# Kernel optimization log

Hardware: AMD Instinct MI355X
Metric: run time of the kernel (lower is better)

The kernel has to match this reference:

```python
import jax, jax.numpy as jnp
import numpy as np

NEG_SLOPE = 0.2  # PyG GATConv default negative_slope
N_NODES = 10000
N_EDGES = 320000
IN_CH = 512
HID = 128
HEADS = 4
N_CLASSES = 2


def gat_conv(x, src, dst, n, W, att_src, att_dst, bias, concat):
    """PyG-style GATConv (shared weights for src/dst, eval mode: no dropout)."""
    H, C = att_src.shape
    h = (x @ W).reshape(-1, H, C)                      # [N, H, C]
    a_src = jnp.sum(h * att_src[None], axis=-1)        # [N, H]
    a_dst = jnp.sum(h * att_dst[None], axis=-1)        # [N, H]
    e = a_src[src] + a_dst[dst]                        # [E, H]
    e = jnp.where(e > 0, e, NEG_SLOPE * e)             # LeakyReLU
    # numerically stable softmax over incoming edges of each dst node
    m = jax.ops.segment_max(e, dst, num_segments=n)    # [N, H]
    m = jnp.where(jnp.isfinite(m), m, 0.0)
    ex = jnp.exp(e - m[dst])
    denom = jax.ops.segment_sum(ex, dst, num_segments=n)
    alpha = ex / (denom[dst] + 1e-16)                  # [E, H]
    out = jax.ops.segment_sum(alpha[:, :, None] * h[src], dst, num_segments=n)  # [N,H,C]
    if concat:
        out = out.reshape(n, H * C)
    else:
        out = out.mean(axis=1)
    return out + bias


def setup_inputs() -> dict:
    key = jax.random.key(0)
    ks = jax.random.split(key, 8)
    x = jax.random.normal(ks[0], (N_NODES, IN_CH), dtype=jnp.float32)
    edge_index = jax.random.randint(ks[1], (2, N_EDGES), 0, N_NODES, dtype=jnp.int32)
    s1 = 1.0 / np.sqrt(IN_CH)
    s2 = 1.0 / np.sqrt(HEADS * HID)
    return {
        "x": x,
        "edge_index": edge_index,
        "W1": jax.random.normal(ks[2], (IN_CH, HEADS * HID), dtype=jnp.float32) * s1,
        "att_src1": jax.random.normal(ks[3], (HEADS, HID), dtype=jnp.float32) * s2,
        "att_dst1": jax.random.normal(ks[4], (HEADS, HID), dtype=jnp.float32) * s2,
        "b1": jnp.zeros((HEADS * HID,), dtype=jnp.float32),
        "W2": jax.random.normal(ks[5], (HEADS * HID, N_CLASSES), dtype=jnp.float32) * s2,
        "att_src2": jax.random.normal(ks[6], (1, N_CLASSES), dtype=jnp.float32),
        "att_dst2": jax.random.normal(ks[7], (1, N_CLASSES), dtype=jnp.float32),
        "b2": jnp.zeros((N_CLASSES,), dtype=jnp.float32),
    }


def reference(x, edge_index, W1, att_src1, att_dst1, b1, W2, att_src2, att_dst2, b2):
    n = x.shape[0]
    loop = jnp.arange(n, dtype=edge_index.dtype)       # PyG add_self_loops=True
    src = jnp.concatenate([edge_index[0], loop])
    dst = jnp.concatenate([edge_index[1], loop])
    h = gat_conv(x, src, dst, n, W1, att_src1, att_dst1, b1, concat=True)
    h = jax.nn.elu(h)
    out = gat_conv(h, src, dst, n, W2, att_src2, att_dst2, b2, concat=False)
    return out
```

## Files before the change

### kernel.cpp

```cpp
#include <hip/hip_runtime.h>
#include <hip/hip_bf16.h>

#define N_NODES 10000
#define N_EDGES 320000
#define E_TOT   330000
#define IN_CH   512
#define F1      512
#define HID     128
#define HEADS   4
#define SLOTS   128

typedef __attribute__((ext_vector_type(8))) short bf16x8;
typedef __attribute__((ext_vector_type(4))) float f32x4;

__device__ __forceinline__ float lo16(unsigned u) { return __uint_as_float(u << 16); }
__device__ __forceinline__ float hi16(unsigned u) { return __uint_as_float(u & 0xffff0000u); }
__device__ __forceinline__ unsigned short bfbits(float f) {
    __hip_bfloat16 h = __float2bfloat16(f);
    return *(unsigned short*)&h;
}

__global__ void k_prep(const float* __restrict__ x, unsigned short* __restrict__ xb,
                       const float* __restrict__ w1, unsigned short* __restrict__ w1t,
                       int* __restrict__ zbase,
                       const int* __restrict__ src, const int* __restrict__ dst,
                       int* __restrict__ cnt, int* __restrict__ slots) {
    __shared__ float tile[64][65];
    int b = blockIdx.x;
    int t = threadIdx.x;
    if (b < 5000) {
        int idx = b * 256 + t;
        float4 v = ((const float4*)x)[idx];
        ushort4 u;
        u.x = bfbits(v.x); u.y = bfbits(v.y); u.z = bfbits(v.z); u.w = bfbits(v.w);
        ((ushort4*)xb)[idx] = u;
    } else if (b < 5064) {
        int bb = b - 5000;
        int bi = bb >> 3, bj = bb & 7;
        int r0 = t >> 6, col = t & 63;
#pragma unroll
        for (int p = 0; p < 16; ++p) {
            int row = p * 4 + r0;
            tile[row][col] = w1[(size_t)(bi * 64 + row) * 512 + bj * 64 + col];
        }
        __syncthreads();
#pragma unroll
        for (int p = 0; p < 16; ++p) {
            int row = p * 4 + r0;
            w1t[(size_t)(bj * 64 + row) * 512 + bi * 64 + col] = bfbits(tile[col][row]);
        }
    } else if (b < 5377) {
        int idx = (b - 5064) * 256 + t;
        if (idx < 80000) zbase[idx] = 0;
    } else {
        int e = (b - 5377) * 256 + t;
        if (e < E_TOT) {
            int d, s;
            if (e < N_EDGES) { d = dst[e]; s = src[e]; } else { d = e - N_EDGES; s = d; }
            int pos = atomicAdd(&cnt[d], 1);
            if (pos < SLOTS) slots[d * SLOTS + pos] = s;
        }
    }
}

__global__ __launch_bounds__(256) void k_gemm1(const __hip_bfloat16* __restrict__ xb,
                                               const __hip_bfloat16* __restrict__ w1t,
                                               const float* __restrict__ as_vec,
                                               const float* __restrict__ ad_vec,
                                               __hip_bfloat16* __restrict__ h1b,
                                               float* __restrict__ a_src,
                                               float* __restrict__ a_dst) {
    int wid = blockIdx.x * 4 + (threadIdx.x >> 6);
    int lane = threadIdx.x & 63;
    int tm = wid >> 3, tn = wid & 7;
    int col16 = lane & 15, quad = lane >> 4;
    int klo = quad * 8;
    int r0g = tm * 32;
    const __hip_bfloat16* a0p = xb + (size_t)min(r0g + col16, N_NODES - 1) * IN_CH + klo;
    const __hip_bfloat16* a1p = xb + (size_t)min(r0g + 16 + col16, N_NODES - 1) * IN_CH + klo;
    const __hip_bfloat16* bp  = w1t + (size_t)(tn * 64 + col16) * IN_CH + klo;
    f32x4 acc[2][4] = {};
    bf16x8 a0c = *(const bf16x8*)(a0p);
    bf16x8 a1c = *(const bf16x8*)(a1p);
    bf16x8 bc[4];
#pragma unroll
    for (int ct = 0; ct < 4; ++ct) bc[ct] = *(const bf16x8*)(bp + (size_t)(ct * 16) * IN_CH);
#pragma unroll
    for (int kt = 0; kt < IN_CH; kt += 32) {
        bf16x8 a0n, a1n, bn[4];
        if (kt + 32 < IN_CH) {
            a0n = *(const bf16x8*)(a0p + kt + 32);
            a1n = *(const bf16x8*)(a1p + kt + 32);
#pragma unroll
            for (int ct = 0; ct < 4; ++ct)
                bn[ct] = *(const bf16x8*)(bp + (size_t)(ct * 16) * IN_CH + kt + 32);
        }
#pragma unroll
        for (int ct = 0; ct < 4; ++ct) {
            acc[0][ct] = __builtin_amdgcn_mfma_f32_16x16x32_bf16(a0c, bc[ct], acc[0][ct], 0, 0, 0);
            acc[1][ct] = __builtin_amdgcn_mfma_f32_16x16x32_bf16(a1c, bc[ct], acc[1][ct], 0, 0, 0);
        }
        if (kt + 32 < IN_CH) {
            a0c = a0n; a1c = a1n;
#pragma unroll
            for (int ct = 0; ct < 4; ++ct) bc[ct] = bn[ct];
        }
    }
    int h_w = tn >> 1;
    float asv[4], adv[4];
#pragma unroll
    for (int ct = 0; ct < 4; ++ct) {
        int c = tn * 64 + ct * 16 + col16;
        asv[ct] = as_vec[c];
        adv[ct] = ad_vec[c];
    }
#pragma unroll
    for (int rt = 0; rt < 2; ++rt) {
#pragma unroll
        for (int reg = 0; reg < 4; ++reg) {
            int row = r0g + rt * 16 + quad * 4 + reg;
            float ps = 0.f, pd = 0.f;
            bool ok = row < N_NODES;
#pragma unroll
            for (int ct = 0; ct < 4; ++ct) {
                float v = acc[rt][ct][reg];
                ps += v * asv[ct];
                pd += v * adv[ct];
                if (ok) h1b[(size_t)row * F1 + tn * 64 + ct * 16 + col16] = __float2bfloat16(v);
            }
#pragma unroll
            for (int off = 1; off <= 8; off <<= 1) {
                ps += __shfl_xor(ps, off);
                pd += __shfl_xor(pd, off);
            }
            if (col16 == 0 && ok) {
                atomicAdd(&a_src[row * HEADS + h_w], ps);
                atomicAdd(&a_dst[row * HEADS + h_w], pd);
            }
        }
    }
}

__global__ __launch_bounds__(256) void k_aggr1(const __hip_bfloat16* __restrict__ h1b,
                                               const float* __restrict__ a_src,
                                               const float* __restrict__ a_dst,
                                               const int* __restrict__ cnt,
                                               const int* __restrict__ slots,
                                               const float* __restrict__ b1,
                                               const float* __restrict__ w2,
                                               const float* __restrict__ as2,
                                               const float* __restrict__ ad2,
                                               float* __restrict__ h2,
                                               float* __restrict__ a_src2,
                                               float* __restrict__ a_dst2) {
    int n = blockIdx.x * 4 + (threadIdx.x >> 6);
    int lane = threadIdx.x & 63;
    int h = lane >> 4;
    int cn = min(cnt[n], SLOTS);
    const int* sl = slots + n * SLOTS;
    float adst = a_dst[n * HEADS + h];
    float dsum = 0.f;
    float acc[8] = {};
    const __hip_bfloat16* hb = h1b + lane * 8;
    for (int i = 0; i < cn; i += 8) {
        int s[8];
        float msk[8];
        uint4 d[8];
        float w[8];
#pragma unroll
        for (int j = 0; j < 8; ++j) {
            int idx = i + j;
            msk[j] = (idx < cn) ? 1.f : 0.f;
            s[j] = sl[min(idx, cn - 1)];
        }
#pragma unroll
        for (int j = 0; j < 8; ++j) d[j] = *(const uint4*)(hb + (size_t)s[j] * F1);
#pragma unroll
        for (int j = 0; j < 8; ++j) {
            float e = a_src[s[j] * HEADS + h] + adst;
            e = fmaxf(e, 0.2f * e);
            w[j] = msk[j] * __expf(e);
            dsum += w[j];
        }
#pragma unroll
        for (int j = 0; j < 8; ++j) {
            acc[0] += w[j] * lo16(d[j].x); acc[1] += w[j] * hi16(d[j].x);
            acc[2] += w[j] * lo16(d[j].y); acc[3] += w[j] * hi16(d[j].y);
            acc[4] += w[j] * lo16(d[j].z); acc[5] += w[j] * hi16(d[j].z);
            acc[6] += w[j] * lo16(d[j].w); acc[7] += w[j] * hi16(d[j].w);
        }
    }
    float inv = 1.f / (dsum + 1e-16f);
    int c0 = lane * 8;
    float ps0 = 0.f, ps1 = 0.f;
#pragma unroll
    for (int j = 0; j < 8; ++j) {
        float v = acc[j] * inv + b1[c0 + j];
        v = v > 0.f ? v : __expf(v) - 1.f;
        ps0 += v * w2[(c0 + j) * 2 + 0];
        ps1 += v * w2[(c0 + j) * 2 + 1];
    }
#pragma unroll
    for (int off = 1; off <= 32; off <<= 1) {
        ps0 += __shfl_xor(ps0, off);
        ps1 += __shfl_xor(ps1, off);
    }
    if (lane == 0) {
        h2[n * 2 + 0] = ps0;
        h2[n * 2 + 1] = ps1;
        a_src2[n] = ps0 * as2[0] + ps1 * as2[1];
        a_dst2[n] = ps0 * ad2[0] + ps1 * ad2[1];
    }
}

__global__ __launch_bounds__(256) void k_aggr2(const float* __restrict__ h2,
                                               const float* __restrict__ a_src2,
                                               const float* __restrict__ a_dst2,
                                               const int* __restrict__ cnt,
                                               const int* __restrict__ slots,
                                               const float* __restrict__ b2,
                                               float* __restrict__ out) {
    int lane = threadIdx.x & 63;
    int sub = lane >> 4, slot = lane & 15;
    int n = blockIdx.x * 16 + (threadIdx.x >> 6) * 4 + sub;
    int cn = min(cnt[n], SLOTS);
    const int* sl = slots + n * SLOTS;
    float adst = a_dst2[n];
    float dsum = 0.f, acc0 = 0.f, acc1 = 0.f;
    for (int i = slot; i < cn; i += 16) {
        int s = sl[i];
        float e = a_src2[s] + adst;
        e = fmaxf(e, 0.2f * e);
        float w = __expf(e);
        dsum += w;
        acc0 += w * h2[s * 2 + 0];
        acc1 += w * h2[s * 2 + 1];
    }
#pragma unroll
    for (int off = 1; off <= 8; off <<= 1) {
        dsum += __shfl_xor(dsum, off);
        acc0 += __shfl_xor(acc0, off);
        acc1 += __shfl_xor(acc1, off);
    }
    if (slot == 0) {
        float inv = 1.f / (dsum + 1e-16f);
        out[n * 2 + 0] = acc0 * inv + b2[0];
        out[n * 2 + 1] = acc1 * inv + b2[1];
    }
}

extern "C" void kernel_launch(void* const* d_in, const int* in_sizes, int n_in,
                              void* d_out, int out_size, void* d_ws, size_t ws_size,
                              hipStream_t stream) {
    const float* x   = (const float*)d_in[0];
    const int*   ei  = (const int*)d_in[1];
    const float* W1  = (const float*)d_in[2];
    const float* as1 = (const float*)d_in[3];
    const float* ad1 = (const float*)d_in[4];
    const float* b1  = (const float*)d_in[5];
    const float* W2  = (const float*)d_in[6];
    const float* as2 = (const float*)d_in[7];
    const float* ad2 = (const float*)d_in[8];
    const float* b2  = (const float*)d_in[9];

    char* ws = (char*)d_ws;
    __hip_bfloat16* h1b = (__hip_bfloat16*)(ws);
    __hip_bfloat16* xb  = (__hip_bfloat16*)(ws + 10240000);
    __hip_bfloat16* w1t = (__hip_bfloat16*)(ws + 20480000);
    const size_t S = 21004288;
    float* a_src1 = (float*)(ws + S);
    float* a_dst1 = (float*)(ws + S + 160000);
    int*   cnt    = (int*)(ws + S + 320000);
    int*   slots  = (int*)(ws + S + 360000);
    float* h2     = (float*)(ws + S + 5480000);
    float* a_src2 = (float*)(ws + S + 5560000);
    float* a_dst2 = (float*)(ws + S + 5600000);

    const int* srcArr = ei;
    const int* dstArr = ei + N_EDGES;

    hipMemsetAsync(cnt, 0, N_NODES * sizeof(int), stream);
    k_prep<<<5377 + 1290, 256, 0, stream>>>(x, (unsigned short*)xb, W1,
                                            (unsigned short*)w1t, (int*)a_src1,
                                            srcArr, dstArr, cnt, slots);
    k_gemm1<<<626, 256, 0, stream>>>(xb, w1t, as1, ad1, h1b, a_src1, a_dst1);
    k_aggr1<<<N_NODES / 4, 256, 0, stream>>>(h1b, a_src1, a_dst1, cnt, slots, b1,
                                             W2, as2, ad2, h2, a_src2, a_dst2);
    k_aggr2<<<N_NODES / 16, 256, 0, stream>>>(h2, a_src2, a_dst2, cnt, slots, b2,
                                              (float*)d_out);
}
```

Before: 188.8 us.

## Overlap edge bucketing with GEMM, shrink GEMM tiles, prefetch gathers in aggregation

Edge slot bucketing moves out of the prep kernel and into extra blocks of the GEMM launch, and the cnt array is now zeroed by the prep kernel's zero range (extended to 90000 ints) instead of a separate memset. The GEMM per-wave tile drops from 32 rows to 16, which doubles the block count and removes the row clamping. The layer-1 aggregation software-pipelines its neighbor gathers, prefetching the next batch's features and attention scores and the following batch's indices with vector loads. This trades more registers and GEMM B-operand reloads for more latency hiding. It also depends on cnt sitting contiguously after a_src1/a_dst1 so the zeroing covers it.

```diff
diff --git a/kernel.cpp b/kernel.cpp
--- a/kernel.cpp
+++ b/kernel.cpp
@@ -22,9 +22,7 @@
 
 __global__ void k_prep(const float* __restrict__ x, unsigned short* __restrict__ xb,
                        const float* __restrict__ w1, unsigned short* __restrict__ w1t,
-                       int* __restrict__ zbase,
-                       const int* __restrict__ src, const int* __restrict__ dst,
-                       int* __restrict__ cnt, int* __restrict__ slots) {
+                       int* __restrict__ zbase) {
     __shared__ float tile[64][65];
     int b = blockIdx.x;
     int t = threadIdx.x;
@@ -49,59 +47,61 @@
             int row = p * 4 + r0;
             w1t[(size_t)(bj * 64 + row) * 512 + bi * 64 + col] = bfbits(tile[col][row]);
         }
-    } else if (b < 5377) {
+    } else {
         int idx = (b - 5064) * 256 + t;
-        if (idx < 80000) zbase[idx] = 0;
-    } else {
-        int e = (b - 5377) * 256 + t;
-        if (e < E_TOT) {
-            int d, s;
-            if (e < N_EDGES) { d = dst[e]; s = src[e]; } else { d = e - N_EDGES; s = d; }
-            int pos = atomicAdd(&cnt[d], 1);
-            if (pos < SLOTS) slots[d * SLOTS + pos] = s;
-        }
-    }
-}
-
+        if (idx < 90000) zbase[idx] = 0;
+    }
+}
+
+#define GEMM_BLKS 1250
 __global__ __launch_bounds__(256) void k_gemm1(const __hip_bfloat16* __restrict__ xb,
                                                const __hip_bfloat16* __restrict__ w1t,
                                                const float* __restrict__ as_vec,
                                                const float* __restrict__ ad_vec,
                                                __hip_bfloat16* __restrict__ h1b,
                                                float* __restrict__ a_src,
-                                               float* __restrict__ a_dst) {
+                                               float* __restrict__ a_dst,
+                                               const int* __restrict__ src,
+                                               const int* __restrict__ dst,
+                                               int* __restrict__ cnt,
+                                               int* __restrict__ slots) {
+    if (blockIdx.x >= GEMM_BLKS) {
+        int e = (blockIdx.x - GEMM_BLKS) * 256 + threadIdx.x;
+        if (e < E_TOT) {
+            int d, s;
+            if (e < N_EDGES) { d = dst[e]; s = src[e]; } else { d = e - N_EDGES; s = d; }
+            int pos = atomicAdd(&cnt[d], 1);
+            if (pos < SLOTS) slots[d * SLOTS + pos] = s;
+        }
+        return;
+    }
     int wid = blockIdx.x * 4 + (threadIdx.x >> 6);
     int lane = threadIdx.x & 63;
     int tm = wid >> 3, tn = wid & 7;
     int col16 = lane & 15, quad = lane >> 4;
     int klo = quad * 8;
-    int r0g = tm * 32;
-    const __hip_bfloat16* a0p = xb + (size_t)min(r0g + col16, N_NODES - 1) * IN_CH + klo;
-    const __hip_bfloat16* a1p = xb + (size_t)min(r0g + 16 + col16, N_NODES - 1) * IN_CH + klo;
-    const __hip_bfloat16* bp  = w1t + (size_t)(tn * 64 + col16) * IN_CH + klo;
-    f32x4 acc[2][4] = {};
-    bf16x8 a0c = *(const bf16x8*)(a0p);
-    bf16x8 a1c = *(const bf16x8*)(a1p);
+    int r0g = tm * 16;
+    const __hip_bfloat16* ap = xb + (size_t)(r0g + col16) * IN_CH + klo;
+    const __hip_bfloat16* bp = w1t + (size_t)(tn * 64 + col16) * IN_CH + klo;
+    f32x4 acc[4] = {};
+    bf16x8 ac = *(const bf16x8*)(ap);
     bf16x8 bc[4];
 #pragma unroll
     for (int ct = 0; ct < 4; ++ct) bc[ct] = *(const bf16x8*)(bp + (size_t)(ct * 16) * IN_CH);
 #pragma unroll
     for (int kt = 0; kt < IN_CH; kt += 32) {
-        bf16x8 a0n, a1n, bn[4];
+        bf16x8 an, bn[4];
         if (kt + 32 < IN_CH) {
-            a0n = *(const bf16x8*)(a0p + kt + 32);
-            a1n = *(const bf16x8*)(a1p + kt + 32);
+            an = *(const bf16x8*)(ap + kt + 32);
 #pragma unroll
             for (int ct = 0; ct < 4; ++ct)
                 bn[ct] = *(const bf16x8*)(bp + (size_t)(ct * 16) * IN_CH + kt + 32);
         }
 #pragma unroll
-        for (int ct = 0; ct < 4; ++ct) {
-            acc[0][ct] = __builtin_amdgcn_mfma_f32_16x16x32_bf16(a0c, bc[ct], acc[0][ct], 0, 0, 0);
-            acc[1][ct] = __builtin_amdgcn_mfma_f32_16x16x32_bf16(a1c, bc[ct], acc[1][ct], 0, 0, 0);
-        }
+        for (int ct = 0; ct < 4; ++ct)
+            acc[ct] = __builtin_amdgcn_mfma_f32_16x16x32_bf16(ac, bc[ct], acc[ct], 0, 0, 0);
         if (kt + 32 < IN_CH) {
-            a0c = a0n; a1c = a1n;
+            ac = an;
 #pragma unroll
             for (int ct = 0; ct < 4; ++ct) bc[ct] = bn[ct];
         }
@@ -115,28 +115,24 @@
         adv[ct] = ad_vec[c];
     }
 #pragma unroll
-    for (int rt = 0; rt < 2; ++rt) {
-#pragma unroll
-        for (int reg = 0; reg < 4; ++reg) {
-            int row = r0g + rt * 16 + quad * 4 + reg;
-            float ps = 0.f, pd = 0.f;
-            bool ok = row < N_NODES;
-#pragma unroll
-            for (int ct = 0; ct < 4; ++ct) {
-                float v = acc[rt][ct][reg];
-                ps += v * asv[ct];
-                pd += v * adv[ct];
-                if (ok) h1b[(size_t)row * F1 + tn * 64 + ct * 16 + col16] = __float2bfloat16(v);
-            }
-#pragma unroll
-            for (int off = 1; off <= 8; off <<= 1) {
-                ps += __shfl_xor(ps, off);
-                pd += __shfl_xor(pd, off);
-            }
-            if (col16 == 0 && ok) {
-                atomicAdd(&a_src[row * HEADS + h_w], ps);
-                atomicAdd(&a_dst[row * HEADS + h_w], pd);
-            }
+    for (int reg = 0; reg < 4; ++reg) {
+        int row = r0g + quad * 4 + reg;
+        float ps = 0.f, pd = 0.f;
+#pragma unroll
+        for (int ct = 0; ct < 4; ++ct) {
+            float v = acc[ct][reg];
+            ps += v * asv[ct];
+            pd += v * adv[ct];
+            h1b[(size_t)row * F1 + tn * 64 + ct * 16 + col16] = __float2bfloat16(v);
+        }
+#pragma unroll
+        for (int off = 1; off <= 8; off <<= 1) {
+            ps += __shfl_xor(ps, off);
+            pd += __shfl_xor(pd, off);
+        }
+        if (col16 == 0) {
+            atomicAdd(&a_src[row * HEADS + h_w], ps);
+            atomicAdd(&a_dst[row * HEADS + h_w], pd);
         }
     }
 }
@@ -162,32 +158,60 @@
     float dsum = 0.f;
     float acc[8] = {};
     const __hip_bfloat16* hb = h1b + lane * 8;
-    for (int i = 0; i < cn; i += 8) {
-        int s[8];
-        float msk[8];
-        uint4 d[8];
+    int nb = (cn + 7) >> 3;
+
+    int sB[8], sC[8] = {0, 0, 0, 0, 0, 0, 0, 0};
+    float avA[8], avB[8];
+    uint4 dA[8], dB[8];
+#pragma unroll
+    for (int j = 0; j < 8; ++j) sB[j] = sl[min(j, cn - 1)];
+#pragma unroll
+    for (int j = 0; j < 8; ++j) avA[j] = a_src[sB[j] * HEADS + h];
+#pragma unroll
+    for (int j = 0; j < 8; ++j) dA[j] = *(const uint4*)(hb + (size_t)sB[j] * F1);
+#pragma unroll
+    for (int j = 0; j < 8; ++j) sB[j] = sl[min(8 + j, cn - 1)];
+
+    for (int b = 0; b < nb; ++b) {
+        int i = b << 3;
+        bool more = (b + 1) < nb;
+        if (b + 2 < nb) {
+            int i2 = i + 16;
+            if (i2 + 8 <= cn) {
+                int4 u0 = *(const int4*)(sl + i2);
+                int4 u1 = *(const int4*)(sl + i2 + 4);
+                sC[0] = u0.x; sC[1] = u0.y; sC[2] = u0.z; sC[3] = u0.w;
+                sC[4] = u1.x; sC[5] = u1.y; sC[6] = u1.z; sC[7] = u1.w;
+            } else {
+#pragma unroll
+                for (int j = 0; j < 8; ++j) sC[j] = sl[min(i2 + j, cn - 1)];
+            }
+        }
+        if (more) {
+#pragma unroll
+            for (int j = 0; j < 8; ++j) avB[j] = a_src[sB[j] * HEADS + h];
+#pragma unroll
+            for (int j = 0; j < 8; ++j) dB[j] = *(const uint4*)(hb + (size_t)sB[j] * F1);
+        }
         float w[8];
 #pragma unroll
         for (int j = 0; j < 8; ++j) {
-            int idx = i + j;
-            msk[j] = (idx < cn) ? 1.f : 0.f;
-            s[j] = sl[min(idx, cn - 1)];
-        }
-#pragma unroll
-        for (int j = 0; j < 8; ++j) d[j] = *(const uint4*)(hb + (size_t)s[j] * F1);
+            float e = avA[j] + adst;
+            e = fmaxf(e, 0.2f * e);
+            float ww = __expf(e);
+            w[j] = (i + j < cn) ? ww : 0.f;
+            dsum += w[j];
+        }
 #pragma unroll
         for (int j = 0; j < 8; ++j) {
-            float e = a_src[s[j] * HEADS + h] + adst;
-            e = fmaxf(e, 0.2f * e);
-            w[j] = msk[j] * __expf(e);
-            dsum += w[j];
-        }
-#pragma unroll
-        for (int j = 0; j < 8; ++j) {
-            acc[0] += w[j] * lo16(d[j].x); acc[1] += w[j] * hi16(d[j].x);
-            acc[2] += w[j] * lo16(d[j].y); acc[3] += w[j] * hi16(d[j].y);
-            acc[4] += w[j] * lo16(d[j].z); acc[5] += w[j] * hi16(d[j].z);
-            acc[6] += w[j] * lo16(d[j].w); acc[7] += w[j] * hi16(d[j].w);
+            acc[0] += w[j] * lo16(dA[j].x); acc[1] += w[j] * hi16(dA[j].x);
+            acc[2] += w[j] * lo16(dA[j].y); acc[3] += w[j] * hi16(dA[j].y);
+            acc[4] += w[j] * lo16(dA[j].z); acc[5] += w[j] * hi16(dA[j].z);
+            acc[6] += w[j] * lo16(dA[j].w); acc[7] += w[j] * hi16(dA[j].w);
+        }
+        if (more) {
+#pragma unroll
+            for (int j = 0; j < 8; ++j) { avA[j] = avB[j]; dA[j] = dB[j]; sB[j] = sC[j]; }
         }
     }
     float inv = 1.f / (dsum + 1e-16f);
@@ -279,11 +303,11 @@
     const int* srcArr = ei;
     const int* dstArr = ei + N_EDGES;
 
-    hipMemsetAsync(cnt, 0, N_NODES * sizeof(int), stream);
-    k_prep<<<5377 + 1290, 256, 0, stream>>>(x, (unsigned short*)xb, W1,
-                                            (unsigned short*)w1t, (int*)a_src1,
-                                            srcArr, dstArr, cnt, slots);
-    k_gemm1<<<626, 256, 0, stream>>>(xb, w1t, as1, ad1, h1b, a_src1, a_dst1);
+    k_prep<<<5064 + 352, 256, 0, stream>>>(x, (unsigned short*)xb, W1,
+                                           (unsigned short*)w1t, (int*)a_src1);
+    k_gemm1<<<GEMM_BLKS + 1290, 256, 0, stream>>>(xb, w1t, as1, ad1, h1b,
+                                                  a_src1, a_dst1,
+                                                  srcArr, dstArr, cnt, slots);
     k_aggr1<<<N_NODES / 4, 256, 0, stream>>>(h1b, a_src1, a_dst1, cnt, slots, b1,
                                              W2, as2, ad2, h2, a_src2, a_dst2);
     k_aggr2<<<N_NODES / 16, 256, 0, stream>>>(h2, a_src2, a_dst2, cnt, slots, b2,
```

After: 200.0 us. 1.06x slower.
